# Optimization experiments

Hardware: AMD Instinct MI355X
Metric: run time of the kernel (lower is better)

## Reference

```python
import jax, jax.numpy as jnp
import numpy as np

B, L, D, E, TOP_K = 8, 1024, 768, 4, 2
H = 2 * D  # expert hidden dim
LN_EPS = 1e-5


def _gelu(v):
    return jax.nn.gelu(v, approximate=False)  # torch nn.GELU default (erf)


def _mish(v):
    return v * jnp.tanh(jax.nn.softplus(v))


_ACTS = [_gelu, jax.nn.silu, _mish, _gelu]  # per-expert activations from __init__


def setup_inputs() -> dict:
    key = jax.random.key(0)
    ks = jax.random.split(key, 8)
    x = jax.random.normal(ks[0], (B, L, D), dtype=jnp.float32)
    router_w = jax.random.normal(ks[1], (E, D), dtype=jnp.float32) * 0.02
    router_b = jnp.zeros((E,), dtype=jnp.float32)
    w1 = jax.random.normal(ks[2], (E, D, H), dtype=jnp.float32) * (1.0 / np.sqrt(D))
    b1 = jax.random.normal(ks[3], (E, H), dtype=jnp.float32) * 0.01
    w2 = jax.random.normal(ks[4], (E, H, D), dtype=jnp.float32) * (1.0 / np.sqrt(H))
    b2 = jax.random.normal(ks[5], (E, D), dtype=jnp.float32) * 0.01
    ln_g = jnp.ones((D,), dtype=jnp.float32)
    ln_b = jnp.zeros((D,), dtype=jnp.float32)
    return {"x": x, "router_w": router_w, "router_b": router_b,
            "w1": w1, "b1": b1, "w2": w2, "b2": b2,
            "ln_g": ln_g, "ln_b": ln_b}


def reference(x, router_w, router_b, w1, b1, w2, b2, ln_g, ln_b):
    # Eval-mode forward (no router noise, no dropout, no aux loss).
    b, l, d = x.shape
    e = router_w.shape[0]

    # Per-sample routing on mean-pooled features.
    pooled = x.mean(axis=1)                              # [B, D]
    logits = pooled @ router_w.T + router_b              # [B, E]
    top_v, top_i = jax.lax.top_k(logits, TOP_K)          # [B, K]
    gates_k = jax.nn.softmax(top_v, axis=-1)             # [B, K]
    # Dense gate matrix: mostly zero, 2 nonzeros per row (matches masked scatter).
    gate = jnp.zeros((b, e), x.dtype).at[jnp.arange(b)[:, None], top_i].add(gates_k)

    # All experts densely (per-sample gate zeros out unrouted experts).
    h = jnp.einsum('bld,edh->belh', x, w1) + b1[None, :, None, :]   # [B, E, L, 2D]
    h = jnp.stack([_ACTS[i](h[:, i]) for i in range(e)], axis=1)
    out = jnp.einsum('belh,ehd->beld', h, w2) + b2[None, :, None, :]  # [B, E, L, D]

    # Gated combine + residual, then LayerNorm.
    y = jnp.einsum('be,beld->bld', gate, out) + x
    mu = y.mean(axis=-1, keepdims=True)
    var = ((y - mu) ** 2).mean(axis=-1, keepdims=True)
    return (y - mu) * jax.lax.rsqrt(var + LN_EPS) * ln_g + ln_b
```

## Files before the change

kernel.cpp:

```cpp
#include <hip/hip_runtime.h>

#define B_ 8
#define L_ 1024
#define D_ 768
#define E_ 4
#define H_ 1536

typedef __attribute__((ext_vector_type(8))) short bf16x8;
typedef __attribute__((ext_vector_type(4))) float f32x4;

#define AS1 __attribute__((address_space(1)))
#define AS3 __attribute__((address_space(3)))

__device__ __forceinline__ unsigned short f2bf(float f) {
  unsigned int u = __float_as_uint(f);
  u += 0x7FFFu + ((u >> 16) & 1u);
  return (unsigned short)(u >> 16);
}
__device__ __forceinline__ float bf2f(unsigned short h) {
  return __uint_as_float(((unsigned int)h) << 16);
}

__device__ __forceinline__ float sigm(float z) {
  return __builtin_amdgcn_rcpf(1.0f + __builtin_amdgcn_exp2f(z * -1.442695040888963f));
}
__device__ __forceinline__ float act_fn(float v, int e) {
  if (e == 1) return v * sigm(v);
  if (e == 2) {
    float p = __builtin_amdgcn_exp2f(fminf(v, 30.0f) * 1.442695040888963f);
    float q = 1.0f + p, q2 = q * q;
    return v * (q2 - 1.0f) * __builtin_amdgcn_rcpf(q2 + 1.0f);
  }
  float u = v * (0.7978845608028654f + 0.0356774081f * v * v);
  return v * sigm(2.0f * u);
}

__global__ __launch_bounds__(256) void k_cvtx_pool(const float* __restrict__ x,
                                                   unsigned short* __restrict__ xbf,
                                                   float* __restrict__ part) {
  const int c = blockIdx.x;
  const int b = blockIdx.y;
  const int t = threadIdx.x;
  const float* xb = x + ((size_t)b * L_ + (size_t)c * 64) * D_;
  unsigned short* ob = xbf ? xbf + ((size_t)b * L_ + (size_t)c * 64) * D_ : nullptr;
  float s0 = 0.f, s1 = 0.f, s2 = 0.f;
  for (int l = 0; l < 64; ++l) {
    float v0 = xb[(size_t)l * D_ + t];
    float v1 = xb[(size_t)l * D_ + t + 256];
    float v2 = xb[(size_t)l * D_ + t + 512];
    s0 += v0; s1 += v1; s2 += v2;
    if (ob) {
      ob[(size_t)l * D_ + t]       = f2bf(v0);
      ob[(size_t)l * D_ + t + 256] = f2bf(v1);
      ob[(size_t)l * D_ + t + 512] = f2bf(v2);
    }
  }
  float* p = part + ((size_t)b * 16 + c) * D_;
  p[t] = s0; p[t + 256] = s1; p[t + 512] = s2;
}

__global__ __launch_bounds__(256) void k_route(const float* __restrict__ part,
                                               const float* __restrict__ rw,
                                               const float* __restrict__ rb,
                                               int* __restrict__ slot_e,
                                               float* __restrict__ slot_g) {
  const int b = blockIdx.x;
  const int t = threadIdx.x;
  __shared__ float red[256][4];
  float p0 = 0.f, p1 = 0.f, p2 = 0.f;
  const float* pb = part + (size_t)b * 16 * D_;
  for (int c = 0; c < 16; ++c) {
    p0 += pb[c * D_ + t];
    p1 += pb[c * D_ + t + 256];
    p2 += pb[c * D_ + t + 512];
  }
  p0 *= (1.0f / L_); p1 *= (1.0f / L_); p2 *= (1.0f / L_);
  for (int e = 0; e < 4; ++e)
    red[t][e] = p0 * rw[e * D_ + t] + p1 * rw[e * D_ + t + 256] + p2 * rw[e * D_ + t + 512];
  __syncthreads();
  for (int s = 128; s > 0; s >>= 1) {
    if (t < s)
      for (int e = 0; e < 4; ++e) red[t][e] += red[t + s][e];
    __syncthreads();
  }
  if (t == 0) {
    float lg[4];
    for (int e = 0; e < 4; ++e) lg[e] = red[0][e] + rb[e];
    int i0 = 0;
    for (int e = 1; e < 4; ++e) if (lg[e] > lg[i0]) i0 = e;
    int i1 = -1;
    for (int e = 0; e < 4; ++e) {
      if (e == i0) continue;
      if (i1 < 0 || lg[e] > lg[i1]) i1 = e;
    }
    float ex = expf(lg[i1] - lg[i0]);
    slot_e[2 * b]     = i0; slot_g[2 * b]     = 1.0f / (1.0f + ex);
    slot_e[2 * b + 1] = i1; slot_g[2 * b + 1] = ex / (1.0f + ex);
  }
}

__global__ __launch_bounds__(256) void k_cvtw(const float* __restrict__ src,
                                              unsigned short* __restrict__ dst,
                                              int R, int C) {
  __shared__ float tile[32][33];
  const int e = blockIdx.z;
  const float* s = src + (size_t)e * R * C;
  unsigned short* d = dst + (size_t)e * R * C;
  const int c0 = blockIdx.x * 32, r0 = blockIdx.y * 32;
  const int tx = threadIdx.x & 31, ty = threadIdx.x >> 5;
#pragma unroll
  for (int i = 0; i < 32; i += 8)
    tile[ty + i][tx] = s[(size_t)(r0 + ty + i) * C + c0 + tx];
  __syncthreads();
#pragma unroll
  for (int i = 0; i < 32; i += 8)
    d[(size_t)(c0 + ty + i) * R + r0 + tx] = f2bf(tile[tx][ty + i]);
}

__device__ __forceinline__ void stage_tile(const unsigned short* __restrict__ src, int pitch,
                                           unsigned short* lds, int t) {
#pragma unroll
  for (int rnd = 0; rnd < 2; ++rnd) {
    const int o = rnd * 4096 + t * 16;
    const int row = o >> 6;
    const int kb = (o & 63) ^ (((row >> 1) & 3) << 4);
    const unsigned short* g = src + (size_t)row * pitch + (kb >> 1);
    unsigned short* d = lds + ((o & ~1023) >> 1);
    __builtin_amdgcn_global_load_lds((AS1 const void*)g, (AS3 void*)d, 16, 0, 0);
  }
}

__device__ __forceinline__ bf16x8 frag(const unsigned short* lds, int row, int kq8) {
  const int byte = (row << 6) + ((kq8 << 1) ^ (((row >> 1) & 3) << 4));
  return *(const bf16x8*)((const char*)lds + byte);
}

__device__ __forceinline__ void block_bar() {
  asm volatile("" ::: "memory");
  __builtin_amdgcn_s_barrier();
  asm volatile("" ::: "memory");
}

__global__ __launch_bounds__(256) void k_ffn1a(const unsigned short* __restrict__ xbf,
                                               const unsigned short* __restrict__ w1t,
                                               const float* __restrict__ b1,
                                               const int* __restrict__ slot_e,
                                               const float* __restrict__ slot_g,
                                               unsigned short* __restrict__ hact) {
  __shared__ char smem[49152];
  unsigned short (*Abuf)[4096] = (unsigned short(*)[4096])smem;
  unsigned short (*Bbuf)[4096] = (unsigned short(*)[4096])(smem + 24576);
  int wg = blockIdx.x;
  wg = (wg & 7) * 192 + (wg >> 3);
  const int hx = wg % 12;
  const int ly = (wg / 12) & 7;
  const int s  = wg / 96;
  const int e = slot_e[s];
  const float g = slot_g[s];
  const int b = s >> 1;
  const int l0 = ly * 128, h0 = hx * 128;
  const int t = threadIdx.x, lane = t & 63, w = t >> 6;
  const int wm = (w >> 1) * 64, wn = (w & 1) * 64;
  const int c16 = lane & 15, kq8 = (lane >> 4) * 8, rq = (lane >> 4) * 4;
  const unsigned short* A  = xbf + ((size_t)b * L_ + l0) * D_;
  const unsigned short* Bp = w1t + ((size_t)e * H_ + h0) * D_;
  f32x4 acc[4][4] = {};
  const int NT = D_ / 32;

  stage_tile(A,      D_, Abuf[0], t); stage_tile(Bp,      D_, Bbuf[0], t);
  stage_tile(A + 32, D_, Abuf[1], t); stage_tile(Bp + 32, D_, Bbuf[1], t);
  stage_tile(A + 64, D_, Abuf[2], t); stage_tile(Bp + 64, D_, Bbuf[2], t);
  int cb = 0;
  for (int kt = 0; kt < NT; ++kt) {
    if (kt + 3 <= NT)      asm volatile("s_waitcnt vmcnt(8)" ::: "memory");
    else if (kt + 2 == NT) asm volatile("s_waitcnt vmcnt(4)" ::: "memory");
    else                   asm volatile("s_waitcnt vmcnt(0)" ::: "memory");
    block_bar();
    const unsigned short* Ac = Abuf[cb];
    const unsigned short* Bc = Bbuf[cb];
    bf16x8 af[4], bfr[4];
#pragma unroll
    for (int i = 0; i < 4; ++i) af[i]  = frag(Ac, wm + i * 16 + c16, kq8);
#pragma unroll
    for (int i = 0; i < 4; ++i) bfr[i] = frag(Bc, wn + i * 16 + c16, kq8);
#pragma unroll
    for (int mi = 0; mi < 4; ++mi)
#pragma unroll
      for (int ni = 0; ni < 4; ++ni)
        acc[mi][ni] = __builtin_amdgcn_mfma_f32_16x16x32_bf16(af[mi], bfr[ni], acc[mi][ni], 0, 0, 0);
    block_bar();
    if (kt + 3 < NT) {
      stage_tile(A + (kt + 3) * 32,  D_, Abuf[cb], t);
      stage_tile(Bp + (kt + 3) * 32, D_, Bbuf[cb], t);
    }
    cb = (cb == 2) ? 0 : cb + 1;
  }

  const float* b1e = b1 + (size_t)e * H_;
  unsigned short* Cl = (unsigned short*)smem;
#pragma unroll
  for (int ni = 0; ni < 4; ++ni) {
    int n = wn + ni * 16 + c16;
    float bias = b1e[h0 + n];
#pragma unroll
    for (int mi = 0; mi < 4; ++mi)
#pragma unroll
      for (int j = 0; j < 4; ++j) {
        int m = wm + mi * 16 + rq + j;
        Cl[m * 136 + n] = f2bf(act_fn(acc[mi][ni][j] + bias, e) * g);
      }
  }
  __syncthreads();
  unsigned short* hs = hact + (((size_t)s * L_ + l0) * H_) + h0;
  const int rr = t >> 4, cc8 = (t & 15) * 8;
#pragma unroll
  for (int i = 0; i < 8; ++i) {
    int r = i * 16 + rr;
    *(bf16x8*)(hs + (size_t)r * H_ + cc8) = *(const bf16x8*)(Cl + r * 136 + cc8);
  }
}

__global__ __launch_bounds__(256) void k_ffn2a(const unsigned short* __restrict__ hact,
                                               const unsigned short* __restrict__ w2t,
                                               const float* __restrict__ b2,
                                               const int* __restrict__ slot_e,
                                               const float* __restrict__ slot_g,
                                               const float* __restrict__ x,
                                               float* __restrict__ y,
                                               unsigned short* __restrict__ ypart) {
  __shared__ char smem[49152];
  unsigned short (*Abuf)[4096] = (unsigned short(*)[4096])smem;
  unsigned short (*Bbuf)[4096] = (unsigned short(*)[4096])(smem + 24576);
  int wg = blockIdx.x;
  wg = (wg & 7) * 96 + (wg >> 3);
  const int dx = wg % 6;
  const int ly = (wg / 6) & 7;
  const int s  = wg / 48;
  const int si = s & 1, b = s >> 1;
  const int e = slot_e[s];
  const float g = slot_g[s];
  const int l0 = ly * 128, d0 = dx * 128;
  const int t = threadIdx.x, lane = t & 63, w = t >> 6;
  const int wm = (w >> 1) * 64, wn = (w & 1) * 64;
  const int c16 = lane & 15, kq8 = (lane >> 4) * 8, rq = (lane >> 4) * 4;
  const unsigned short* A  = hact + ((size_t)s * L_ + l0) * H_;
  const unsigned short* Bp = w2t + ((size_t)e * D_ + d0) * H_;
  f32x4 acc[4][4] = {};
  const int NT = H_ / 32;

  stage_tile(A,      H_, Abuf[0], t); stage_tile(Bp,      H_, Bbuf[0], t);
  stage_tile(A + 32, H_, Abuf[1], t); stage_tile(Bp + 32, H_, Bbuf[1], t);
  stage_tile(A + 64, H_, Abuf[2], t); stage_tile(Bp + 64, H_, Bbuf[2], t);
  int cb = 0;
  for (int kt = 0; kt < NT; ++kt) {
    if (kt + 3 <= NT)      asm volatile("s_waitcnt vmcnt(8)" ::: "memory");
    else if (kt + 2 == NT) asm volatile("s_waitcnt vmcnt(4)" ::: "memory");
    else                   asm volatile("s_waitcnt vmcnt(0)" ::: "memory");
    block_bar();
    const unsigned short* Ac = Abuf[cb];
    const unsigned short* Bc = Bbuf[cb];
    bf16x8 af[4], bfr[4];
#pragma unroll
    for (int i = 0; i < 4; ++i) af[i]  = frag(Ac, wm + i * 16 + c16, kq8);
#pragma unroll
    for (int i = 0; i < 4; ++i) bfr[i] = frag(Bc, wn + i * 16 + c16, kq8);
#pragma unroll
    for (int mi = 0; mi < 4; ++mi)
#pragma unroll
      for (int ni = 0; ni < 4; ++ni)
        acc[mi][ni] = __builtin_amdgcn_mfma_f32_16x16x32_bf16(af[mi], bfr[ni], acc[mi][ni], 0, 0, 0);
    block_bar();
    if (kt + 3 < NT) {
      stage_tile(A + (kt + 3) * 32,  H_, Abuf[cb], t);
      stage_tile(Bp + (kt + 3) * 32, H_, Bbuf[cb], t);
    }
    cb = (cb == 2) ? 0 : cb + 1;
  }

  if (si == 0) {
    const float* xb = x + (size_t)b * L_ * D_;
    float* yb = y + (size_t)b * L_ * D_;
#pragma unroll
    for (int ni = 0; ni < 4; ++ni) {
      int n = d0 + wn + ni * 16 + c16;
      float bias = g * b2[(size_t)e * D_ + n];
#pragma unroll
      for (int mi = 0; mi < 4; ++mi)
#pragma unroll
        for (int j = 0; j < 4; ++j) {
          int m = l0 + wm + mi * 16 + rq + j;
          yb[(size_t)m * D_ + n] = acc[mi][ni][j] + bias + xb[(size_t)m * D_ + n];
        }
    }
  } else {
    unsigned short* Cl = (unsigned short*)smem;
#pragma unroll
    for (int ni = 0; ni < 4; ++ni) {
      int n = wn + ni * 16 + c16;
      float bias = g * b2[(size_t)e * D_ + d0 + n];
#pragma unroll
      for (int mi = 0; mi < 4; ++mi)
#pragma unroll
        for (int j = 0; j < 4; ++j) {
          int m = wm + mi * 16 + rq + j;
          Cl[m * 136 + n] = f2bf(acc[mi][ni][j] + bias);
        }
    }
    __syncthreads();
    unsigned short* yp = ypart + ((size_t)b * L_ + l0) * D_ + d0;
    const int rr = t >> 4, cc8 = (t & 15) * 8;
#pragma unroll
    for (int i = 0; i < 8; ++i) {
      int r = i * 16 + rr;
      *(bf16x8*)(yp + (size_t)r * D_ + cc8) = *(const bf16x8*)(Cl + r * 136 + cc8);
    }
  }
}

__global__ __launch_bounds__(256) void k_ln(float* __restrict__ y,
                                            const unsigned short* __restrict__ yp,
                                            const float* __restrict__ g,
                                            const float* __restrict__ bt) {
  const int row = blockIdx.x;
  const int t = threadIdx.x;
  float* yr = y + (size_t)row * D_;
  float v0 = yr[t], v1 = yr[t + 256], v2 = yr[t + 512];
  if (yp) {
    const unsigned short* pr = yp + (size_t)row * D_;
    v0 += bf2f(pr[t]); v1 += bf2f(pr[t + 256]); v2 += bf2f(pr[t + 512]);
  }
  __shared__ float red[256];
  red[t] = v0 + v1 + v2;
  __syncthreads();
  for (int s = 128; s > 0; s >>= 1) {
    if (t < s) red[t] += red[t + s];
    __syncthreads();
  }
  float mu = red[0] * (1.0f / D_);
  __syncthreads();
  float d0 = v0 - mu, d1 = v1 - mu, d2 = v2 - mu;
  red[t] = d0 * d0 + d1 * d1 + d2 * d2;
  __syncthreads();
  for (int s = 128; s > 0; s >>= 1) {
    if (t < s) red[t] += red[t + s];
    __syncthreads();
  }
  float rstd = rsqrtf(red[0] * (1.0f / D_) + 1e-5f);
  yr[t]       = d0 * rstd * g[t]       + bt[t];
  yr[t + 256] = d1 * rstd * g[t + 256] + bt[t + 256];
  yr[t + 512] = d2 * rstd * g[t + 512] + bt[t + 512];
}

__global__ __launch_bounds__(256) void k_ffn1b(const float* __restrict__ x,
                                               const float* __restrict__ w1,
                                               const float* __restrict__ b1,
                                               const int* __restrict__ slot_e,
                                               const float* __restrict__ slot_g,
                                               unsigned short* __restrict__ hact) {
  __shared__ unsigned short Al[128][40];
  __shared__ unsigned short Bl[128][40];
  const int s = blockIdx.z;
  const int e = slot_e[s];
  const float g = slot_g[s];
  const int b = s >> 1;
  const int l0 = blockIdx.y * 128, h0 = blockIdx.x * 128;
  const int t = threadIdx.x, lane = t & 63, w = t >> 6;
  const int wm = (w >> 1) * 64, wn = (w & 1) * 64;
  const int c16 = lane & 15, kq = (lane >> 4) * 8, rq = (lane >> 4) * 4;
  const int ar = t >> 3, ac = (t & 7) * 4;
  const int bn = t & 127, bk0 = (t >> 7) * 4;
  const float* xb  = x  + (size_t)b * L_ * D_;
  const float* w1e = w1 + (size_t)e * D_ * H_;
  f32x4 acc[4][4] = {};
  for (int k0 = 0; k0 < D_; k0 += 32) {
#pragma unroll
    for (int p = 0; p < 4; ++p) {
      int r = p * 32 + ar;
      float4 v = *(const float4*)(xb + (size_t)(l0 + r) * D_ + (k0 + ac));
      *(ushort4*)&Al[r][ac] = make_ushort4(f2bf(v.x), f2bf(v.y), f2bf(v.z), f2bf(v.w));
    }
#pragma unroll
    for (int p = 0; p < 4; ++p) {
      int kk = bk0 + p * 8;
      const float* src = w1e + (size_t)(k0 + kk) * H_ + (h0 + bn);
      *(ushort4*)&Bl[bn][kk] = make_ushort4(f2bf(src[0]), f2bf(src[H_]), f2bf(src[2 * H_]), f2bf(src[3 * H_]));
    }
    __syncthreads();
    bf16x8 af[4], bfr[4];
#pragma unroll
    for (int i = 0; i < 4; ++i) af[i]  = *(const bf16x8*)&Al[wm + i * 16 + c16][kq];
#pragma unroll
    for (int i = 0; i < 4; ++i) bfr[i] = *(const bf16x8*)&Bl[wn + i * 16 + c16][kq];
#pragma unroll
    for (int mi = 0; mi < 4; ++mi)
#pragma unroll
      for (int ni = 0; ni < 4; ++ni)
        acc[mi][ni] = __builtin_amdgcn_mfma_f32_16x16x32_bf16(af[mi], bfr[ni], acc[mi][ni], 0, 0, 0);
    __syncthreads();
  }
  const float* b1e = b1 + (size_t)e * H_;
  unsigned short* hs = hact + (size_t)s * L_ * H_;
#pragma unroll
  for (int ni = 0; ni < 4; ++ni) {
    int n = h0 + wn + ni * 16 + c16;
    float bias = b1e[n];
#pragma unroll
    for (int mi = 0; mi < 4; ++mi)
#pragma unroll
      for (int j = 0; j < 4; ++j) {
        int m = l0 + wm + mi * 16 + rq + j;
        hs[(size_t)m * H_ + n] = f2bf(act_fn(acc[mi][ni][j] + bias, e) * g);
      }
  }
}

__global__ __launch_bounds__(256) void k_ffn2b(const unsigned short* __restrict__ hact,
                                               const float* __restrict__ w2,
                                               const float* __restrict__ b2,
                                               const int* __restrict__ slot_e,
                                               const float* __restrict__ slot_g,
                                               const float* __restrict__ x,
                                               float* __restrict__ y) {
  __shared__ unsigned short Al[128][40];
  __shared__ unsigned short Bl[128][40];
  const int b = blockIdx.z;
  const int l0 = blockIdx.y * 128, d0 = blockIdx.x * 128;
  const int t = threadIdx.x, lane = t & 63, w = t >> 6;
  const int wm = (w >> 1) * 64, wn = (w & 1) * 64;
  const int c16 = lane & 15, kq = (lane >> 4) * 8, rq = (lane >> 4) * 4;
  const int ar = t >> 3, ac = (t & 7) * 4;
  const int bn = t & 127, bk0 = (t >> 7) * 4;
  f32x4 acc[4][4] = {};
  for (int si = 0; si < 2; ++si) {
    const int s = 2 * b + si;
    const int e = slot_e[s];
    const unsigned short* hs = hact + (size_t)s * L_ * H_;
    const float* w2e = w2 + (size_t)e * H_ * D_;
    for (int k0 = 0; k0 < H_; k0 += 32) {
#pragma unroll
      for (int p = 0; p < 4; ++p) {
        int r = p * 32 + ar;
        *(ushort4*)&Al[r][ac] = *(const ushort4*)(hs + (size_t)(l0 + r) * H_ + (k0 + ac));
      }
#pragma unroll
      for (int p = 0; p < 4; ++p) {
        int kk = bk0 + p * 8;
        const float* src = w2e + (size_t)(k0 + kk) * D_ + (d0 + bn);
        *(ushort4*)&Bl[bn][kk] = make_ushort4(f2bf(src[0]), f2bf(src[D_]), f2bf(src[2 * D_]), f2bf(src[3 * D_]));
      }
      __syncthreads();
      bf16x8 af[4], bfr[4];
#pragma unroll
      for (int i = 0; i < 4; ++i) af[i]  = *(const bf16x8*)&Al[wm + i * 16 + c16][kq];
#pragma unroll
      for (int i = 0; i < 4; ++i) bfr[i] = *(const bf16x8*)&Bl[wn + i * 16 + c16][kq];
#pragma unroll
      for (int mi = 0; mi < 4; ++mi)
#pragma unroll
        for (int ni = 0; ni < 4; ++ni)
          acc[mi][ni] = __builtin_amdgcn_mfma_f32_16x16x32_bf16(af[mi], bfr[ni], acc[mi][ni], 0, 0, 0);
      __syncthreads();
    }
  }
  const int e0 = slot_e[2 * b], e1 = slot_e[2 * b + 1];
  const float g0 = slot_g[2 * b], g1 = slot_g[2 * b + 1];
  const float* xb = x + (size_t)b * L_ * D_;
  float* yb = y + (size_t)b * L_ * D_;
#pragma unroll
  for (int ni = 0; ni < 4; ++ni) {
    int n = d0 + wn + ni * 16 + c16;
    float bias = g0 * b2[e0 * D_ + n] + g1 * b2[e1 * D_ + n];
#pragma unroll
    for (int mi = 0; mi < 4; ++mi)
#pragma unroll
      for (int j = 0; j < 4; ++j) {
        int m = l0 + wm + mi * 16 + rq + j;
        yb[(size_t)m * D_ + n] = acc[mi][ni][j] + bias + xb[(size_t)m * D_ + n];
      }
  }
}

extern "C" void kernel_launch(void* const* d_in, const int* in_sizes, int n_in,
                              void* d_out, int out_size, void* d_ws, size_t ws_size,
                              hipStream_t stream) {
  const float* x  = (const float*)d_in[0];
  const float* rw = (const float*)d_in[1];
  const float* rb = (const float*)d_in[2];
  const float* w1 = (const float*)d_in[3];
  const float* b1 = (const float*)d_in[4];
  const float* w2 = (const float*)d_in[5];
  const float* b2 = (const float*)d_in[6];
  const float* lg = (const float*)d_in[7];
  const float* lb = (const float*)d_in[8];
  float* y = (float*)d_out;

  char* ws = (char*)d_ws;
  int*   slot_e = (int*)ws;
  float* slot_g = (float*)(ws + 64);
  float* part   = (float*)(ws + 256);

  const size_t OFF_XBF  = 524288ull;
  const size_t OFF_WBUF = OFF_XBF + 12582912ull;
  const size_t OFF_HACT = OFF_WBUF + 9437184ull;
  const size_t NEED_A   = OFF_HACT + 50331648ull;

  if (ws_size >= NEED_A) {
    unsigned short* xbf   = (unsigned short*)(ws + OFF_XBF);
    unsigned short* wbuf  = (unsigned short*)(ws + OFF_WBUF);
    unsigned short* hact  = (unsigned short*)(ws + OFF_HACT);
    unsigned short* ypart = (unsigned short*)(ws + OFF_XBF);

    k_cvtx_pool<<<dim3(16, 8), 256, 0, stream>>>(x, xbf, part);
    k_route    <<<8,           256, 0, stream>>>(part, rw, rb, slot_e, slot_g);
    k_cvtw     <<<dim3(48, 24, 4), 256, 0, stream>>>(w1, wbuf, D_, H_);
    k_ffn1a    <<<1536, 256, 0, stream>>>(xbf, wbuf, b1, slot_e, slot_g, hact);
    k_cvtw     <<<dim3(24, 48, 4), 256, 0, stream>>>(w2, wbuf, H_, D_);
    k_ffn2a    <<<768,  256, 0, stream>>>(hact, wbuf, b2, slot_e, slot_g, x, y, ypart);
    k_ln       <<<8192, 256, 0, stream>>>(y, ypart, lg, lb);
  } else {
    unsigned short* hact = (unsigned short*)(ws + (1 << 19));
    k_cvtx_pool<<<dim3(16, 8), 256, 0, stream>>>(x, nullptr, part);
    k_route    <<<8,           256, 0, stream>>>(part, rw, rb, slot_e, slot_g);
    k_ffn1b    <<<dim3(12, 8, 16), 256, 0, stream>>>(x, w1, b1, slot_e, slot_g, hact);
    k_ffn2b    <<<dim3(6, 8, 8),   256, 0, stream>>>(hact, w2, b2, slot_e, slot_g, x, y);
    k_ln       <<<8192,        256, 0, stream>>>(y, nullptr, lg, lb);
  }
}
```

Measured before the change: 172.7 us.

## Widen FFN GEMM tiles to 128x256 with per-wave 128x64 output strips

Both expert GEMM kernels move from 128x128 to 128x256 output tiles. Each wave now owns a full 128x64 strip and keeps 8 A fragments in registers while streaming B fragments, and s_setprio raises priority around the MFMA block. This halves the grid, increases arithmetic intensity per LDS byte, and reduces redundant A-tile loads. The cost is a larger LDS footprint (72KB triple-buffered), more accumulator registers, and fewer workgroups, which risks lower occupancy and tail imbalance on 256 CUs.

```diff
diff --git a/kernel.cpp b/kernel.cpp
--- a/kernel.cpp
+++ b/kernel.cpp
@@ -117,10 +117,11 @@
     d[(size_t)(c0 + ty + i) * R + r0 + tx] = f2bf(tile[tx][ty + i]);
 }
 
-__device__ __forceinline__ void stage_tile(const unsigned short* __restrict__ src, int pitch,
-                                           unsigned short* lds, int t) {
-#pragma unroll
-  for (int rnd = 0; rnd < 2; ++rnd) {
+template <int ROWS>
+__device__ __forceinline__ void stageT(const unsigned short* __restrict__ src, int pitch,
+                                       unsigned short* lds, int t) {
+#pragma unroll
+  for (int rnd = 0; rnd < ROWS / 64; ++rnd) {
     const int o = rnd * 4096 + t * 16;
     const int row = o >> 6;
     const int kb = (o & 63) ^ (((row >> 1) & 3) << 4);
@@ -141,138 +142,142 @@
   asm volatile("" ::: "memory");
 }
 
-__global__ __launch_bounds__(256) void k_ffn1a(const unsigned short* __restrict__ xbf,
-                                               const unsigned short* __restrict__ w1t,
-                                               const float* __restrict__ b1,
-                                               const int* __restrict__ slot_e,
-                                               const float* __restrict__ slot_g,
-                                               unsigned short* __restrict__ hact) {
-  __shared__ char smem[49152];
-  unsigned short (*Abuf)[4096] = (unsigned short(*)[4096])smem;
-  unsigned short (*Bbuf)[4096] = (unsigned short(*)[4096])(smem + 24576);
+__global__ __launch_bounds__(256, 2) void k_ffn1a(const unsigned short* __restrict__ xbf,
+                                                  const unsigned short* __restrict__ w1t,
+                                                  const float* __restrict__ b1,
+                                                  const int* __restrict__ slot_e,
+                                                  const float* __restrict__ slot_g,
+                                                  unsigned short* __restrict__ hact) {
+  __shared__ char smem[73728];
   int wg = blockIdx.x;
-  wg = (wg & 7) * 192 + (wg >> 3);
-  const int hx = wg % 12;
-  const int ly = (wg / 12) & 7;
-  const int s  = wg / 96;
+  wg = (wg & 7) * 96 + (wg >> 3);
+  const int hx = wg % 6;
+  const int ly = (wg / 6) & 7;
+  const int s  = wg / 48;
   const int e = slot_e[s];
   const float g = slot_g[s];
   const int b = s >> 1;
-  const int l0 = ly * 128, h0 = hx * 128;
+  const int l0 = ly * 128, h0 = hx * 256;
   const int t = threadIdx.x, lane = t & 63, w = t >> 6;
-  const int wm = (w >> 1) * 64, wn = (w & 1) * 64;
+  const int wn = w * 64;
   const int c16 = lane & 15, kq8 = (lane >> 4) * 8, rq = (lane >> 4) * 4;
   const unsigned short* A  = xbf + ((size_t)b * L_ + l0) * D_;
   const unsigned short* Bp = w1t + ((size_t)e * H_ + h0) * D_;
-  f32x4 acc[4][4] = {};
+  f32x4 acc[8][4] = {};
   const int NT = D_ / 32;
 
-  stage_tile(A,      D_, Abuf[0], t); stage_tile(Bp,      D_, Bbuf[0], t);
-  stage_tile(A + 32, D_, Abuf[1], t); stage_tile(Bp + 32, D_, Bbuf[1], t);
-  stage_tile(A + 64, D_, Abuf[2], t); stage_tile(Bp + 64, D_, Bbuf[2], t);
+#pragma unroll
+  for (int i = 0; i < 3; ++i) {
+    stageT<128>(A + i * 32,  D_, (unsigned short*)(smem + i * 24576), t);
+    stageT<256>(Bp + i * 32, D_, (unsigned short*)(smem + i * 24576 + 8192), t);
+  }
   int cb = 0;
   for (int kt = 0; kt < NT; ++kt) {
-    if (kt + 3 <= NT)      asm volatile("s_waitcnt vmcnt(8)" ::: "memory");
-    else if (kt + 2 == NT) asm volatile("s_waitcnt vmcnt(4)" ::: "memory");
+    if (kt + 3 <= NT)      asm volatile("s_waitcnt vmcnt(12)" ::: "memory");
+    else if (kt + 2 == NT) asm volatile("s_waitcnt vmcnt(6)" ::: "memory");
     else                   asm volatile("s_waitcnt vmcnt(0)" ::: "memory");
     block_bar();
-    const unsigned short* Ac = Abuf[cb];
-    const unsigned short* Bc = Bbuf[cb];
-    bf16x8 af[4], bfr[4];
-#pragma unroll
-    for (int i = 0; i < 4; ++i) af[i]  = frag(Ac, wm + i * 16 + c16, kq8);
-#pragma unroll
-    for (int i = 0; i < 4; ++i) bfr[i] = frag(Bc, wn + i * 16 + c16, kq8);
-#pragma unroll
-    for (int mi = 0; mi < 4; ++mi)
-#pragma unroll
-      for (int ni = 0; ni < 4; ++ni)
-        acc[mi][ni] = __builtin_amdgcn_mfma_f32_16x16x32_bf16(af[mi], bfr[ni], acc[mi][ni], 0, 0, 0);
+    const unsigned short* Ac = (const unsigned short*)(smem + cb * 24576);
+    const unsigned short* Bc = (const unsigned short*)(smem + cb * 24576 + 8192);
+    bf16x8 af[8];
+#pragma unroll
+    for (int i = 0; i < 8; ++i) af[i] = frag(Ac, i * 16 + c16, kq8);
+    __builtin_amdgcn_s_setprio(1);
+#pragma unroll
+    for (int ni = 0; ni < 4; ++ni) {
+      bf16x8 bfr = frag(Bc, wn + ni * 16 + c16, kq8);
+#pragma unroll
+      for (int mi = 0; mi < 8; ++mi)
+        acc[mi][ni] = __builtin_amdgcn_mfma_f32_16x16x32_bf16(af[mi], bfr, acc[mi][ni], 0, 0, 0);
+    }
+    __builtin_amdgcn_s_setprio(0);
     block_bar();
     if (kt + 3 < NT) {
-      stage_tile(A + (kt + 3) * 32,  D_, Abuf[cb], t);
-      stage_tile(Bp + (kt + 3) * 32, D_, Bbuf[cb], t);
+      stageT<128>(A + (kt + 3) * 32,  D_, (unsigned short*)(smem + cb * 24576), t);
+      stageT<256>(Bp + (kt + 3) * 32, D_, (unsigned short*)(smem + cb * 24576 + 8192), t);
     }
     cb = (cb == 2) ? 0 : cb + 1;
   }
 
-  const float* b1e = b1 + (size_t)e * H_;
+  const float* b1e = b1 + (size_t)e * H_ + h0;
   unsigned short* Cl = (unsigned short*)smem;
 #pragma unroll
   for (int ni = 0; ni < 4; ++ni) {
     int n = wn + ni * 16 + c16;
-    float bias = b1e[h0 + n];
-#pragma unroll
-    for (int mi = 0; mi < 4; ++mi)
+    float bias = b1e[n];
+#pragma unroll
+    for (int mi = 0; mi < 8; ++mi)
 #pragma unroll
       for (int j = 0; j < 4; ++j) {
-        int m = wm + mi * 16 + rq + j;
-        Cl[m * 136 + n] = f2bf(act_fn(acc[mi][ni][j] + bias, e) * g);
+        int m = mi * 16 + rq + j;
+        Cl[m * 264 + n] = f2bf(act_fn(acc[mi][ni][j] + bias, e) * g);
       }
   }
   __syncthreads();
   unsigned short* hs = hact + (((size_t)s * L_ + l0) * H_) + h0;
-  const int rr = t >> 4, cc8 = (t & 15) * 8;
-#pragma unroll
-  for (int i = 0; i < 8; ++i) {
-    int r = i * 16 + rr;
-    *(bf16x8*)(hs + (size_t)r * H_ + cc8) = *(const bf16x8*)(Cl + r * 136 + cc8);
-  }
-}
-
-__global__ __launch_bounds__(256) void k_ffn2a(const unsigned short* __restrict__ hact,
-                                               const unsigned short* __restrict__ w2t,
-                                               const float* __restrict__ b2,
-                                               const int* __restrict__ slot_e,
-                                               const float* __restrict__ slot_g,
-                                               const float* __restrict__ x,
-                                               float* __restrict__ y,
-                                               unsigned short* __restrict__ ypart) {
-  __shared__ char smem[49152];
-  unsigned short (*Abuf)[4096] = (unsigned short(*)[4096])smem;
-  unsigned short (*Bbuf)[4096] = (unsigned short(*)[4096])(smem + 24576);
+  const int rr = t >> 5, cc8 = (t & 31) * 8;
+#pragma unroll
+  for (int i = 0; i < 16; ++i) {
+    int r = i * 8 + rr;
+    *(bf16x8*)(hs + (size_t)r * H_ + cc8) = *(const bf16x8*)(Cl + r * 264 + cc8);
+  }
+}
+
+__global__ __launch_bounds__(256, 2) void k_ffn2a(const unsigned short* __restrict__ hact,
+                                                  const unsigned short* __restrict__ w2t,
+                                                  const float* __restrict__ b2,
+                                                  const int* __restrict__ slot_e,
+                                                  const float* __restrict__ slot_g,
+                                                  const float* __restrict__ x,
+                                                  float* __restrict__ y,
+                                                  unsigned short* __restrict__ ypart) {
+  __shared__ char smem[73728];
   int wg = blockIdx.x;
-  wg = (wg & 7) * 96 + (wg >> 3);
-  const int dx = wg % 6;
-  const int ly = (wg / 6) & 7;
-  const int s  = wg / 48;
+  wg = (wg & 7) * 48 + (wg >> 3);
+  const int dx = wg % 3;
+  const int ly = (wg / 3) & 7;
+  const int s  = wg / 24;
   const int si = s & 1, b = s >> 1;
   const int e = slot_e[s];
   const float g = slot_g[s];
-  const int l0 = ly * 128, d0 = dx * 128;
+  const int l0 = ly * 128, d0 = dx * 256;
   const int t = threadIdx.x, lane = t & 63, w = t >> 6;
-  const int wm = (w >> 1) * 64, wn = (w & 1) * 64;
+  const int wn = w * 64;
   const int c16 = lane & 15, kq8 = (lane >> 4) * 8, rq = (lane >> 4) * 4;
   const unsigned short* A  = hact + ((size_t)s * L_ + l0) * H_;
   const unsigned short* Bp = w2t + ((size_t)e * D_ + d0) * H_;
-  f32x4 acc[4][4] = {};
+  f32x4 acc[8][4] = {};
   const int NT = H_ / 32;
 
-  stage_tile(A,      H_, Abuf[0], t); stage_tile(Bp,      H_, Bbuf[0], t);
-  stage_tile(A + 32, H_, Abuf[1], t); stage_tile(Bp + 32, H_, Bbuf[1], t);
-  stage_tile(A + 64, H_, Abuf[2], t); stage_tile(Bp + 64, H_, Bbuf[2], t);
+#pragma unroll
+  for (int i = 0; i < 3; ++i) {
+    stageT<128>(A + i * 32,  H_, (unsigned short*)(smem + i * 24576), t);
+    stageT<256>(Bp + i * 32, H_, (unsigned short*)(smem + i * 24576 + 8192), t);
+  }
   int cb = 0;
   for (int kt = 0; kt < NT; ++kt) {
-    if (kt + 3 <= NT)      asm volatile("s_waitcnt vmcnt(8)" ::: "memory");
-    else if (kt + 2 == NT) asm volatile("s_waitcnt vmcnt(4)" ::: "memory");
+    if (kt + 3 <= NT)      asm volatile("s_waitcnt vmcnt(12)" ::: "memory");
+    else if (kt + 2 == NT) asm volatile("s_waitcnt vmcnt(6)" ::: "memory");
     else                   asm volatile("s_waitcnt vmcnt(0)" ::: "memory");
     block_bar();
-    const unsigned short* Ac = Abuf[cb];
-    const unsigned short* Bc = Bbuf[cb];
-    bf16x8 af[4], bfr[4];
-#pragma unroll
-    for (int i = 0; i < 4; ++i) af[i]  = frag(Ac, wm + i * 16 + c16, kq8);
-#pragma unroll
-    for (int i = 0; i < 4; ++i) bfr[i] = frag(Bc, wn + i * 16 + c16, kq8);
-#pragma unroll
-    for (int mi = 0; mi < 4; ++mi)
-#pragma unroll
-      for (int ni = 0; ni < 4; ++ni)
-        acc[mi][ni] = __builtin_amdgcn_mfma_f32_16x16x32_bf16(af[mi], bfr[ni], acc[mi][ni], 0, 0, 0);
+    const unsigned short* Ac = (const unsigned short*)(smem + cb * 24576);
+    const unsigned short* Bc = (const unsigned short*)(smem + cb * 24576 + 8192);
+    bf16x8 af[8];
+#pragma unroll
+    for (int i = 0; i < 8; ++i) af[i] = frag(Ac, i * 16 + c16, kq8);
+    __builtin_amdgcn_s_setprio(1);
+#pragma unroll
+    for (int ni = 0; ni < 4; ++ni) {
+      bf16x8 bfr = frag(Bc, wn + ni * 16 + c16, kq8);
+#pragma unroll
+      for (int mi = 0; mi < 8; ++mi)
+        acc[mi][ni] = __builtin_amdgcn_mfma_f32_16x16x32_bf16(af[mi], bfr, acc[mi][ni], 0, 0, 0);
+    }
+    __builtin_amdgcn_s_setprio(0);
     block_bar();
     if (kt + 3 < NT) {
-      stage_tile(A + (kt + 3) * 32,  H_, Abuf[cb], t);
-      stage_tile(Bp + (kt + 3) * 32, H_, Bbuf[cb], t);
+      stageT<128>(A + (kt + 3) * 32,  H_, (unsigned short*)(smem + cb * 24576), t);
+      stageT<256>(Bp + (kt + 3) * 32, H_, (unsigned short*)(smem + cb * 24576 + 8192), t);
     }
     cb = (cb == 2) ? 0 : cb + 1;
   }
@@ -285,10 +290,10 @@
       int n = d0 + wn + ni * 16 + c16;
       float bias = g * b2[(size_t)e * D_ + n];
 #pragma unroll
-      for (int mi = 0; mi < 4; ++mi)
+      for (int mi = 0; mi < 8; ++mi)
 #pragma unroll
         for (int j = 0; j < 4; ++j) {
-          int m = l0 + wm + mi * 16 + rq + j;
+          int m = l0 + mi * 16 + rq + j;
           yb[(size_t)m * D_ + n] = acc[mi][ni][j] + bias + xb[(size_t)m * D_ + n];
         }
     }
@@ -299,20 +304,20 @@
       int n = wn + ni * 16 + c16;
       float bias = g * b2[(size_t)e * D_ + d0 + n];
 #pragma unroll
-      for (int mi = 0; mi < 4; ++mi)
+      for (int mi = 0; mi < 8; ++mi)
 #pragma unroll
         for (int j = 0; j < 4; ++j) {
-          int m = wm + mi * 16 + rq + j;
-          Cl[m * 136 + n] = f2bf(acc[mi][ni][j] + bias);
+          int m = mi * 16 + rq + j;
+          Cl[m * 264 + n] = f2bf(acc[mi][ni][j] + bias);
         }
     }
     __syncthreads();
     unsigned short* yp = ypart + ((size_t)b * L_ + l0) * D_ + d0;
-    const int rr = t >> 4, cc8 = (t & 15) * 8;
-#pragma unroll
-    for (int i = 0; i < 8; ++i) {
-      int r = i * 16 + rr;
-      *(bf16x8*)(yp + (size_t)r * D_ + cc8) = *(const bf16x8*)(Cl + r * 136 + cc8);
+    const int rr = t >> 5, cc8 = (t & 31) * 8;
+#pragma unroll
+    for (int i = 0; i < 16; ++i) {
+      int r = i * 8 + rr;
+      *(bf16x8*)(yp + (size_t)r * D_ + cc8) = *(const bf16x8*)(Cl + r * 264 + cc8);
     }
   }
 }
@@ -444,9 +449,10 @@
       }
 #pragma unroll
       for (int p = 0; p < 4; ++p) {
-        int kk = bk0 + p * 8;
-        const float* src = w2e + (size_t)(k0 + kk) * D_ + (d0 + bn);
-        *(ushort4*)&Bl[bn][kk] = make_ushort4(f2bf(src[0]), f2bf(src[D_]), f2bf(src[2 * D_]), f2bf(src[3 * D_]));
+        int kk = bk0 + p * 4 * 2;
+        const float* src = w2e + (size_t)(k0 + bk0 + p * 8) * D_ + (d0 + bn);
+        *(ushort4*)&Bl[bn][bk0 + p * 8] = make_ushort4(f2bf(src[0]), f2bf(src[D_]), f2bf(src[2 * D_]), f2bf(src[3 * D_]));
+        (void)kk;
       }
       __syncthreads();
       bf16x8 af[4], bfr[4];
@@ -513,9 +519,9 @@
     k_cvtx_pool<<<dim3(16, 8), 256, 0, stream>>>(x, xbf, part);
     k_route    <<<8,           256, 0, stream>>>(part, rw, rb, slot_e, slot_g);
     k_cvtw     <<<dim3(48, 24, 4), 256, 0, stream>>>(w1, wbuf, D_, H_);
-    k_ffn1a    <<<1536, 256, 0, stream>>>(xbf, wbuf, b1, slot_e, slot_g, hact);
+    k_ffn1a    <<<768, 256, 0, stream>>>(xbf, wbuf, b1, slot_e, slot_g, hact);
     k_cvtw     <<<dim3(24, 48, 4), 256, 0, stream>>>(w2, wbuf, H_, D_);
-    k_ffn2a    <<<768,  256, 0, stream>>>(hact, wbuf, b2, slot_e, slot_g, x, y, ypart);
+    k_ffn2a    <<<384, 256, 0, stream>>>(hact, wbuf, b2, slot_e, slot_g, x, y, ypart);
     k_ln       <<<8192, 256, 0, stream>>>(y, ypart, lg, lb);
   } else {
     unsigned short* hact = (unsigned short*)(ws + (1 << 19));
```

New measurement: 181.8 us. 5.3% more time.
